# Optimization experiments

Measured on AMD Instinct MI355X. Metric: run time of the kernel, lower is better.

Reference implementation:

```python
import jax, jax.numpy as jnp
import numpy as np

T, B, I, H = 2048, 4096, 3, 5  # seq_len, batch, input_size, hidden_size (from module)


def setup_inputs() -> dict:
    key = jax.random.key(0)
    ks = jax.random.split(key, 10)
    k = 1.0 / np.sqrt(H)  # torch nn.RNN default init bound
    u = lambda kk, shape: jax.random.uniform(kk, shape, jnp.float32, -k, k)
    return {
        "x": jax.random.normal(ks[0], (T, B, I), jnp.float32),
        "hx": jax.random.normal(ks[1], (2, B, H), jnp.float32),
        "w_ih0": u(ks[2], (H, I)),
        "w_hh0": u(ks[3], (H, H)),
        "b_ih0": u(ks[4], (H,)),
        "b_hh0": u(ks[5], (H,)),
        "w_ih1": u(ks[6], (H, H)),
        "w_hh1": u(ks[7], (H, H)),
        "b_ih1": u(ks[8], (H,)),
        "b_hh1": u(ks[9], (H,)),
    }


def reference(x, hx, w_ih0, w_hh0, b_ih0, b_hh0, w_ih1, w_hh1, b_ih1, b_hh1):
    # Precompute layer-0 input projections for all timesteps in one big GEMM.
    pre0 = jnp.einsum("tbi,hi->tbh", x, w_ih0) + b_ih0  # [T, B, H]

    def step(carry, p0_t):
        h0, h1 = carry
        h0 = jnp.tanh(p0_t + h0 @ w_hh0.T + b_hh0)
        h1 = jnp.tanh(h0 @ w_ih1.T + b_ih1 + h1 @ w_hh1.T + b_hh1)
        return (h0, h1), h1

    (h0_f, h1_f), out = jax.lax.scan(step, (hx[0], hx[1]), pre0)
    h_n = jnp.stack([h0_f, h1_f])  # [2, B, H]
    return out, h_n
```

## Files before the change

### kernel.cpp

```cpp
#include <hip/hip_runtime.h>


typedef float v2f __attribute__((ext_vector_type(2)));

#define SEQ_T 2048
#define BATCH 4096
#define ISZ 3
#define HSZ 5
#define PD 8
#define XSTRIDE (BATCH * ISZ)
#define OSTRIDE (BATCH * HSZ)

template<int K>
__device__ __forceinline__ float qbcast(float v) {
    return __int_as_float(__builtin_amdgcn_mov_dpp(
        __float_as_int(v), K * 0x55, 0xF, 0xF, false));
}

__device__ __forceinline__ float tanh_fast(float a) {
    float e = __builtin_amdgcn_exp2f(a);
    return fmaf(-2.0f, __builtin_amdgcn_rcpf(1.0f + e), 1.0f);
}

__device__ __forceinline__ v2f vsplat(float s) { return (v2f){s, s}; }
__device__ __forceinline__ v2f vfma(float s, v2f w, v2f a) {
    return __builtin_elementwise_fma(vsplat(s), w, a);
}

__global__ __launch_bounds__(64, 1)
void rnn2_regs(const float* __restrict__ x, const float* __restrict__ hx,
               const float* __restrict__ w_ih0, const float* __restrict__ w_hh0,
               const float* __restrict__ b_ih0, const float* __restrict__ b_hh0,
               const float* __restrict__ w_ih1, const float* __restrict__ w_hh1,
               const float* __restrict__ b_ih1, const float* __restrict__ b_hh1,
               float* __restrict__ out)
{
    const int tid = threadIdx.x;
    const int c   = (blockIdx.x * 64 + tid) >> 2;
    const int ja  = tid & 3;
    const float S = 2.8853900817779268f;

    const v2f bias0p = (v2f){ S * (b_ih0[ja] + b_hh0[ja]), S * (b_ih0[4] + b_hh0[4]) };
    const v2f bias1p = (v2f){ S * (b_ih1[ja] + b_hh1[ja]), S * (b_ih1[4] + b_hh1[4]) };
#define LW(W, k, n)  (v2f){ S * W[ja * (n) + (k)], S * W[4 * (n) + (k)] }
    const v2f wi0p0 = LW(w_ih0, 0, ISZ), wi0p1 = LW(w_ih0, 1, ISZ), wi0p2 = LW(w_ih0, 2, ISZ);
    const v2f wh0p0 = LW(w_hh0, 0, HSZ), wh0p1 = LW(w_hh0, 1, HSZ), wh0p2 = LW(w_hh0, 2, HSZ),
              wh0p3 = LW(w_hh0, 3, HSZ), wh0p4 = LW(w_hh0, 4, HSZ);
    const v2f wi1p0 = LW(w_ih1, 0, HSZ), wi1p1 = LW(w_ih1, 1, HSZ), wi1p2 = LW(w_ih1, 2, HSZ),
              wi1p3 = LW(w_ih1, 3, HSZ), wi1p4 = LW(w_ih1, 4, HSZ);
    const v2f wh1p0 = LW(w_hh1, 0, HSZ), wh1p1 = LW(w_hh1, 1, HSZ), wh1p2 = LW(w_hh1, 2, HSZ),
              wh1p3 = LW(w_hh1, 3, HSZ), wh1p4 = LW(w_hh1, 4, HSZ);
#undef LW

    float h0b0 = hx[(size_t)c * HSZ + 0], h0b1 = hx[(size_t)c * HSZ + 1],
          h0b2 = hx[(size_t)c * HSZ + 2], h0b3 = hx[(size_t)c * HSZ + 3],
          h0b4 = hx[(size_t)c * HSZ + 4];
    const size_t hb1 = (size_t)BATCH * HSZ + (size_t)c * HSZ;
    float h1b0 = hx[hb1 + 0], h1b1 = hx[hb1 + 1], h1b2 = hx[hb1 + 2],
          h1b3 = hx[hb1 + 3], h1b4 = hx[hb1 + 4];

    unsigned xoff = (unsigned)c * ISZ;
    float x0a = x[xoff + 0*XSTRIDE], x0b = x[xoff + 0*XSTRIDE + 1], x0c = x[xoff + 0*XSTRIDE + 2];
    float x1a = x[xoff + 1*XSTRIDE], x1b = x[xoff + 1*XSTRIDE + 1], x1c = x[xoff + 1*XSTRIDE + 2];
    float x2a = x[xoff + 2*XSTRIDE], x2b = x[xoff + 2*XSTRIDE + 1], x2c = x[xoff + 2*XSTRIDE + 2];
    float x3a = x[xoff + 3*XSTRIDE], x3b = x[xoff + 3*XSTRIDE + 1], x3c = x[xoff + 3*XSTRIDE + 2];
    float x4a = x[xoff + 4*XSTRIDE], x4b = x[xoff + 4*XSTRIDE + 1], x4c = x[xoff + 4*XSTRIDE + 2];
    float x5a = x[xoff + 5*XSTRIDE], x5b = x[xoff + 5*XSTRIDE + 1], x5c = x[xoff + 5*XSTRIDE + 2];
    float x6a = x[xoff + 6*XSTRIDE], x6b = x[xoff + 6*XSTRIDE + 1], x6c = x[xoff + 6*XSTRIDE + 2];
    float x7a = x[xoff + 7*XSTRIDE], x7b = x[xoff + 7*XSTRIDE + 1], x7c = x[xoff + 7*XSTRIDE + 2];
    xoff += PD * XSTRIDE;

    unsigned ooffA = (unsigned)c * HSZ + (unsigned)ja;
    unsigned ooffB = (unsigned)c * HSZ + 4u;

#define CORE(XV0, XV1, XV2, DOLOAD)                                        \
    {                                                                      \
        const float xv0 = XV0, xv1 = XV1, xv2 = XV2;                       \
        if (DOLOAD) {                                                      \
            XV0 = x[xoff]; XV1 = x[xoff + 1]; XV2 = x[xoff + 2];           \
            xoff += XSTRIDE;                                               \
        }                                                                  \
        v2f a = bias0p, cc = (v2f){0.0f, 0.0f};                            \
        a  = vfma(xv0,  wi0p0, a);                                         \
        cc = vfma(xv1,  wi0p1, cc);                                        \
        a  = vfma(xv2,  wi0p2, a);                                         \
        cc = vfma(h0b0, wh0p0, cc);                                        \
        a  = vfma(h0b1, wh0p1, a);                                         \
        cc = vfma(h0b2, wh0p2, cc);                                        \
        a  = vfma(h0b3, wh0p3, a);                                         \
        cc = vfma(h0b4, wh0p4, cc);                                        \
        a = a + cc;                                                        \
        const float h0nA = tanh_fast(a.x);                                 \
        const float h0nB = tanh_fast(a.y);                                 \
        h0b0 = qbcast<0>(h0nA);                                            \
        h0b1 = qbcast<1>(h0nA);                                            \
        h0b2 = qbcast<2>(h0nA);                                            \
        h0b3 = qbcast<3>(h0nA);                                            \
        h0b4 = h0nB;                                                       \
        v2f d = bias1p, ee = (v2f){0.0f, 0.0f};                            \
        d  = vfma(h0b0, wi1p0, d);                                         \
        ee = vfma(h0b1, wi1p1, ee);                                        \
        d  = vfma(h0b2, wi1p2, d);                                         \
        ee = vfma(h0b3, wi1p3, ee);                                        \
        d  = vfma(h0b4, wi1p4, d);                                         \
        ee = vfma(h1b0, wh1p0, ee);                                        \
        d  = vfma(h1b1, wh1p1, d);                                         \
        ee = vfma(h1b2, wh1p2, ee);                                        \
        d  = vfma(h1b3, wh1p3, d);                                         \
        ee = vfma(h1b4, wh1p4, ee);                                        \
        d = d + ee;                                                        \
        const float h1nA = tanh_fast(d.x);                                 \
        const float h1nB = tanh_fast(d.y);                                 \
        out[ooffA] = h1nA;                                                 \
        out[ooffB] = h1nB;                                                 \
        ooffA += OSTRIDE;                                                  \
        ooffB += OSTRIDE;                                                  \
        h1b0 = qbcast<0>(h1nA);                                            \
        h1b1 = qbcast<1>(h1nA);                                            \
        h1b2 = qbcast<2>(h1nA);                                            \
        h1b3 = qbcast<3>(h1nA);                                            \
        h1b4 = h1nB;                                                       \
    }

    for (int it = 0; it < SEQ_T / PD - 1; ++it) {
        CORE(x0a, x0b, x0c, 1)
        CORE(x1a, x1b, x1c, 1)
        CORE(x2a, x2b, x2c, 1)
        CORE(x3a, x3b, x3c, 1)
        CORE(x4a, x4b, x4c, 1)
        CORE(x5a, x5b, x5c, 1)
        CORE(x6a, x6b, x6c, 1)
        CORE(x7a, x7b, x7c, 1)
    }
    CORE(x0a, x0b, x0c, 0)
    CORE(x1a, x1b, x1c, 0)
    CORE(x2a, x2b, x2c, 0)
    CORE(x3a, x3b, x3c, 0)
    CORE(x4a, x4b, x4c, 0)
    CORE(x5a, x5b, x5c, 0)
    CORE(x6a, x6b, x6c, 0)
    CORE(x7a, x7b, x7c, 0)
#undef CORE

    float* hn = out + (size_t)SEQ_T * BATCH * HSZ;
    hn[(size_t)c * HSZ + 0] = h0b0;
    hn[(size_t)c * HSZ + 1] = h0b1;
    hn[(size_t)c * HSZ + 2] = h0b2;
    hn[(size_t)c * HSZ + 3] = h0b3;
    hn[(size_t)c * HSZ + 4] = h0b4;
    hn[hb1 + 0] = h1b0;
    hn[hb1 + 1] = h1b1;
    hn[hb1 + 2] = h1b2;
    hn[hb1 + 3] = h1b3;
    hn[hb1 + 4] = h1b4;
}

extern "C" void kernel_launch(void* const* d_in, const int* in_sizes, int n_in,
                              void* d_out, int out_size, void* d_ws, size_t ws_size,
                              hipStream_t stream) {
    rnn2_regs<<<(BATCH * 4) / 64, 64, 0, stream>>>(
        (const float*)d_in[0], (const float*)d_in[1],
        (const float*)d_in[2], (const float*)d_in[3],
        (const float*)d_in[4], (const float*)d_in[5],
        (const float*)d_in[6], (const float*)d_in[7],
        (const float*)d_in[8], (const float*)d_in[9],
        (float*)d_out);
}
```

Baseline: 478.0 us.

## Pipeline RNN layers across two wavefronts via shared-memory ring buffer

Splits the two RNN layers onto separate wavefronts in a 128-thread block. Wave 0 computes layer 0 for an 8-step block and writes h0 into a double-buffered LDS ring, while wave 1 consumes the previous block to compute layer 1 and write outputs. The aim is to shorten the serial per-step dependency chain by overlapping the two layers. In exchange it adds a block barrier every 8 steps, LDS traffic, and one extra pipeline stage of latency.

```diff
diff --git a/kernel.cpp b/kernel.cpp
--- a/kernel.cpp
+++ b/kernel.cpp
@@ -7,7 +7,8 @@
 #define BATCH 4096
 #define ISZ 3
 #define HSZ 5
-#define PD 8
+#define TBLK 8
+#define NSUP (SEQ_T / TBLK)
 #define XSTRIDE (BATCH * ISZ)
 #define OSTRIDE (BATCH * HSZ)
 
@@ -16,29 +17,32 @@
     return __int_as_float(__builtin_amdgcn_mov_dpp(
         __float_as_int(v), K * 0x55, 0xF, 0xF, false));
 }
-
 __device__ __forceinline__ float tanh_fast(float a) {
     float e = __builtin_amdgcn_exp2f(a);
     return fmaf(-2.0f, __builtin_amdgcn_rcpf(1.0f + e), 1.0f);
 }
-
 __device__ __forceinline__ v2f vsplat(float s) { return (v2f){s, s}; }
 __device__ __forceinline__ v2f vfma(float s, v2f w, v2f a) {
     return __builtin_elementwise_fma(vsplat(s), w, a);
 }
 
-__global__ __launch_bounds__(64, 1)
-void rnn2_regs(const float* __restrict__ x, const float* __restrict__ hx,
-               const float* __restrict__ w_ih0, const float* __restrict__ w_hh0,
-               const float* __restrict__ b_ih0, const float* __restrict__ b_hh0,
-               const float* __restrict__ w_ih1, const float* __restrict__ w_hh1,
-               const float* __restrict__ b_ih1, const float* __restrict__ b_hh1,
-               float* __restrict__ out)
+__global__ __launch_bounds__(128, 1)
+void rnn2_ppl(const float* __restrict__ x, const float* __restrict__ hx,
+              const float* __restrict__ w_ih0, const float* __restrict__ w_hh0,
+              const float* __restrict__ b_ih0, const float* __restrict__ b_hh0,
+              const float* __restrict__ w_ih1, const float* __restrict__ w_hh1,
+              const float* __restrict__ b_ih1, const float* __restrict__ b_hh1,
+              float* __restrict__ out)
 {
-    const int tid = threadIdx.x;
-    const int c   = (blockIdx.x * 64 + tid) >> 2;
-    const int ja  = tid & 3;
-    const float S = 2.8853900817779268f;
+    __shared__ float ring[2][TBLK][16][10];
+
+    const int tid  = threadIdx.x;
+    const int wid  = tid >> 6;
+    const int lane = tid & 63;
+    const int cl   = lane >> 2;
+    const int ja   = lane & 3;
+    const int c    = blockIdx.x * 16 + cl;
+    const float S  = 2.8853900817779268f;
 
     const v2f bias0p = (v2f){ S * (b_ih0[ja] + b_hh0[ja]), S * (b_ih0[4] + b_hh0[4]) };
     const v2f bias1p = (v2f){ S * (b_ih1[ja] + b_hh1[ja]), S * (b_ih1[4] + b_hh1[4]) };
@@ -68,18 +72,16 @@
     float x5a = x[xoff + 5*XSTRIDE], x5b = x[xoff + 5*XSTRIDE + 1], x5c = x[xoff + 5*XSTRIDE + 2];
     float x6a = x[xoff + 6*XSTRIDE], x6b = x[xoff + 6*XSTRIDE + 1], x6c = x[xoff + 6*XSTRIDE + 2];
     float x7a = x[xoff + 7*XSTRIDE], x7b = x[xoff + 7*XSTRIDE + 1], x7c = x[xoff + 7*XSTRIDE + 2];
-    xoff += PD * XSTRIDE;
+    xoff += TBLK * XSTRIDE;
 
     unsigned ooffA = (unsigned)c * HSZ + (unsigned)ja;
     unsigned ooffB = (unsigned)c * HSZ + 4u;
 
-#define CORE(XV0, XV1, XV2, DOLOAD)                                        \
+#define STEP0(TT, XV0, XV1, XV2)                                           \
     {                                                                      \
         const float xv0 = XV0, xv1 = XV1, xv2 = XV2;                       \
-        if (DOLOAD) {                                                      \
-            XV0 = x[xoff]; XV1 = x[xoff + 1]; XV2 = x[xoff + 2];           \
-            xoff += XSTRIDE;                                               \
-        }                                                                  \
+        XV0 = x[xoff]; XV1 = x[xoff + 1]; XV2 = x[xoff + 2];               \
+        xoff += XSTRIDE;                                                   \
         v2f a = bias0p, cc = (v2f){0.0f, 0.0f};                            \
         a  = vfma(xv0,  wi0p0, a);                                         \
         cc = vfma(xv1,  wi0p1, cc);                                        \
@@ -90,75 +92,103 @@
         a  = vfma(h0b3, wh0p3, a);                                         \
         cc = vfma(h0b4, wh0p4, cc);                                        \
         a = a + cc;                                                        \
-        const float h0nA = tanh_fast(a.x);                                 \
-        const float h0nB = tanh_fast(a.y);                                 \
-        h0b0 = qbcast<0>(h0nA);                                            \
-        h0b1 = qbcast<1>(h0nA);                                            \
-        h0b2 = qbcast<2>(h0nA);                                            \
-        h0b3 = qbcast<3>(h0nA);                                            \
-        h0b4 = h0nB;                                                       \
+        const float nA = tanh_fast(a.x);                                   \
+        const float nB = tanh_fast(a.y);                                   \
+        h0b0 = qbcast<0>(nA);                                              \
+        h0b1 = qbcast<1>(nA);                                              \
+        h0b2 = qbcast<2>(nA);                                              \
+        h0b3 = qbcast<3>(nA);                                              \
+        h0b4 = nB;                                                         \
+        *(v2f*)&wr[TT][cl][ja * 2] = (v2f){nA, nB};                        \
+    }
+
+#define STEP1(TT, DOPRE)                                                   \
+    {                                                                      \
+        const float u0 = g0, u1 = g1, u2 = g2, u3 = g3, u4 = g4;           \
+        if (DOPRE) {                                                       \
+            const float* q = &rd[(TT) + 1][cl][0];                         \
+            g0 = q[0]; g1 = q[2]; g2 = q[4]; g3 = q[6]; g4 = q[1];         \
+        }                                                                  \
         v2f d = bias1p, ee = (v2f){0.0f, 0.0f};                            \
-        d  = vfma(h0b0, wi1p0, d);                                         \
-        ee = vfma(h0b1, wi1p1, ee);                                        \
-        d  = vfma(h0b2, wi1p2, d);                                         \
-        ee = vfma(h0b3, wi1p3, ee);                                        \
-        d  = vfma(h0b4, wi1p4, d);                                         \
+        d  = vfma(u0,   wi1p0, d);                                         \
+        ee = vfma(u1,   wi1p1, ee);                                        \
+        d  = vfma(u2,   wi1p2, d);                                         \
+        ee = vfma(u3,   wi1p3, ee);                                        \
+        d  = vfma(u4,   wi1p4, d);                                         \
         ee = vfma(h1b0, wh1p0, ee);                                        \
         d  = vfma(h1b1, wh1p1, d);                                         \
         ee = vfma(h1b2, wh1p2, ee);                                        \
         d  = vfma(h1b3, wh1p3, d);                                         \
         ee = vfma(h1b4, wh1p4, ee);                                        \
         d = d + ee;                                                        \
-        const float h1nA = tanh_fast(d.x);                                 \
-        const float h1nB = tanh_fast(d.y);                                 \
-        out[ooffA] = h1nA;                                                 \
-        out[ooffB] = h1nB;                                                 \
+        const float nA = tanh_fast(d.x);                                   \
+        const float nB = tanh_fast(d.y);                                   \
+        out[ooffA] = nA;                                                   \
+        out[ooffB] = nB;                                                   \
         ooffA += OSTRIDE;                                                  \
         ooffB += OSTRIDE;                                                  \
-        h1b0 = qbcast<0>(h1nA);                                            \
-        h1b1 = qbcast<1>(h1nA);                                            \
-        h1b2 = qbcast<2>(h1nA);                                            \
-        h1b3 = qbcast<3>(h1nA);                                            \
-        h1b4 = h1nB;                                                       \
+        h1b0 = qbcast<0>(nA);                                              \
+        h1b1 = qbcast<1>(nA);                                              \
+        h1b2 = qbcast<2>(nA);                                              \
+        h1b3 = qbcast<3>(nA);                                              \
+        h1b4 = nB;                                                         \
     }
 
-    for (int it = 0; it < SEQ_T / PD - 1; ++it) {
-        CORE(x0a, x0b, x0c, 1)
-        CORE(x1a, x1b, x1c, 1)
-        CORE(x2a, x2b, x2c, 1)
-        CORE(x3a, x3b, x3c, 1)
-        CORE(x4a, x4b, x4c, 1)
-        CORE(x5a, x5b, x5c, 1)
-        CORE(x6a, x6b, x6c, 1)
-        CORE(x7a, x7b, x7c, 1)
+    for (int si = 0; si <= NSUP; ++si) {
+        __syncthreads();
+        if (wid == 0) {
+            if (si < NSUP) {
+                if (si == NSUP - 1) xoff -= (unsigned)(TBLK * XSTRIDE);
+                float (*wr)[16][10] = ring[si & 1];
+                STEP0(0, x0a, x0b, x0c)
+                STEP0(1, x1a, x1b, x1c)
+                STEP0(2, x2a, x2b, x2c)
+                STEP0(3, x3a, x3b, x3c)
+                STEP0(4, x4a, x4b, x4c)
+                STEP0(5, x5a, x5b, x5c)
+                STEP0(6, x6a, x6b, x6c)
+                STEP0(7, x7a, x7b, x7c)
+            }
+        } else {
+            if (si > 0) {
+                float (*rd)[16][10] = ring[(si - 1) & 1];
+                float g0, g1, g2, g3, g4;
+                { const float* q = &rd[0][cl][0];
+                  g0 = q[0]; g1 = q[2]; g2 = q[4]; g3 = q[6]; g4 = q[1]; }
+                STEP1(0, 1)
+                STEP1(1, 1)
+                STEP1(2, 1)
+                STEP1(3, 1)
+                STEP1(4, 1)
+                STEP1(5, 1)
+                STEP1(6, 1)
+                STEP1(7, 0)
+            }
+        }
     }
-    CORE(x0a, x0b, x0c, 0)
-    CORE(x1a, x1b, x1c, 0)
-    CORE(x2a, x2b, x2c, 0)
-    CORE(x3a, x3b, x3c, 0)
-    CORE(x4a, x4b, x4c, 0)
-    CORE(x5a, x5b, x5c, 0)
-    CORE(x6a, x6b, x6c, 0)
-    CORE(x7a, x7b, x7c, 0)
-#undef CORE
+#undef STEP0
+#undef STEP1
 
     float* hn = out + (size_t)SEQ_T * BATCH * HSZ;
-    hn[(size_t)c * HSZ + 0] = h0b0;
-    hn[(size_t)c * HSZ + 1] = h0b1;
-    hn[(size_t)c * HSZ + 2] = h0b2;
-    hn[(size_t)c * HSZ + 3] = h0b3;
-    hn[(size_t)c * HSZ + 4] = h0b4;
-    hn[hb1 + 0] = h1b0;
-    hn[hb1 + 1] = h1b1;
-    hn[hb1 + 2] = h1b2;
-    hn[hb1 + 3] = h1b3;
-    hn[hb1 + 4] = h1b4;
+    if (wid == 0) {
+        hn[(size_t)c * HSZ + 0] = h0b0;
+        hn[(size_t)c * HSZ + 1] = h0b1;
+        hn[(size_t)c * HSZ + 2] = h0b2;
+        hn[(size_t)c * HSZ + 3] = h0b3;
+        hn[(size_t)c * HSZ + 4] = h0b4;
+    } else {
+        hn[hb1 + 0] = h1b0;
+        hn[hb1 + 1] = h1b1;
+        hn[hb1 + 2] = h1b2;
+        hn[hb1 + 3] = h1b3;
+        hn[hb1 + 4] = h1b4;
+    }
 }
 
 extern "C" void kernel_launch(void* const* d_in, const int* in_sizes, int n_in,
                               void* d_out, int out_size, void* d_ws, size_t ws_size,
                               hipStream_t stream) {
-    rnn2_regs<<<(BATCH * 4) / 64, 64, 0, stream>>>(
+    rnn2_ppl<<<BATCH / 16, 128, 0, stream>>>(
         (const float*)d_in[0], (const float*)d_in[1],
         (const float*)d_in[2], (const float*)d_in[3],
         (const float*)d_in[4], (const float*)d_in[5],
```

After: 535.1 us. 11.9% more time.

## Software-pipeline the two RNN layers across timesteps to shorten the dependency chain

Applied to the files above, without the earlier changes.

Layer 1 of step t-1 is now computed in the same block as layer 0 of step t, since both depend only on h0 from step t-1. This interleaves two independent FMA, exp and rcp chains per iteration and roughly halves the serial critical path per timestep. A prologue runs layer 0 alone and an epilogue finishes the last layer-1 step. Register pressure rises somewhat from the extra live accumulators.

```diff
diff --git a/kernel.cpp b/kernel.cpp
--- a/kernel.cpp
+++ b/kernel.cpp
@@ -7,7 +7,6 @@
 #define BATCH 4096
 #define ISZ 3
 #define HSZ 5
-#define PD 8
 #define XSTRIDE (BATCH * ISZ)
 #define OSTRIDE (BATCH * HSZ)
 
@@ -16,24 +15,18 @@
     return __int_as_float(__builtin_amdgcn_mov_dpp(
         __float_as_int(v), K * 0x55, 0xF, 0xF, false));
 }
-
-__device__ __forceinline__ float tanh_fast(float a) {
-    float e = __builtin_amdgcn_exp2f(a);
-    return fmaf(-2.0f, __builtin_amdgcn_rcpf(1.0f + e), 1.0f);
-}
-
 __device__ __forceinline__ v2f vsplat(float s) { return (v2f){s, s}; }
 __device__ __forceinline__ v2f vfma(float s, v2f w, v2f a) {
     return __builtin_elementwise_fma(vsplat(s), w, a);
 }
 
 __global__ __launch_bounds__(64, 1)
-void rnn2_regs(const float* __restrict__ x, const float* __restrict__ hx,
-               const float* __restrict__ w_ih0, const float* __restrict__ w_hh0,
-               const float* __restrict__ b_ih0, const float* __restrict__ b_hh0,
-               const float* __restrict__ w_ih1, const float* __restrict__ w_hh1,
-               const float* __restrict__ b_ih1, const float* __restrict__ b_hh1,
-               float* __restrict__ out)
+void rnn2_swp(const float* __restrict__ x, const float* __restrict__ hx,
+              const float* __restrict__ w_ih0, const float* __restrict__ w_hh0,
+              const float* __restrict__ b_ih0, const float* __restrict__ b_hh0,
+              const float* __restrict__ w_ih1, const float* __restrict__ w_hh1,
+              const float* __restrict__ b_ih1, const float* __restrict__ b_hh1,
+              float* __restrict__ out)
 {
     const int tid = threadIdx.x;
     const int c   = (blockIdx.x * 64 + tid) >> 2;
@@ -68,18 +61,69 @@
     float x5a = x[xoff + 5*XSTRIDE], x5b = x[xoff + 5*XSTRIDE + 1], x5c = x[xoff + 5*XSTRIDE + 2];
     float x6a = x[xoff + 6*XSTRIDE], x6b = x[xoff + 6*XSTRIDE + 1], x6c = x[xoff + 6*XSTRIDE + 2];
     float x7a = x[xoff + 7*XSTRIDE], x7b = x[xoff + 7*XSTRIDE + 1], x7c = x[xoff + 7*XSTRIDE + 2];
-    xoff += PD * XSTRIDE;
+    xoff += 8 * XSTRIDE;
 
     unsigned ooffA = (unsigned)c * HSZ + (unsigned)ja;
     unsigned ooffB = (unsigned)c * HSZ + 4u;
 
-#define CORE(XV0, XV1, XV2, DOLOAD)                                        \
+#define PAIR(XV0, XV1, XV2, DOLOAD)                                        \
     {                                                                      \
         const float xv0 = XV0, xv1 = XV1, xv2 = XV2;                       \
         if (DOLOAD) {                                                      \
             XV0 = x[xoff]; XV1 = x[xoff + 1]; XV2 = x[xoff + 2];           \
             xoff += XSTRIDE;                                               \
         }                                                                  \
+        v2f a = bias0p, cc = (v2f){0.0f, 0.0f};                            \
+        v2f d = bias1p, ee = (v2f){0.0f, 0.0f};                            \
+        a  = vfma(xv0,  wi0p0, a);                                         \
+        d  = vfma(h0b0, wi1p0, d);                                         \
+        cc = vfma(xv1,  wi0p1, cc);                                        \
+        ee = vfma(h0b1, wi1p1, ee);                                        \
+        a  = vfma(xv2,  wi0p2, a);                                         \
+        d  = vfma(h0b2, wi1p2, d);                                         \
+        cc = vfma(h0b0, wh0p0, cc);                                        \
+        ee = vfma(h0b3, wi1p3, ee);                                        \
+        a  = vfma(h0b1, wh0p1, a);                                         \
+        d  = vfma(h0b4, wi1p4, d);                                         \
+        cc = vfma(h0b2, wh0p2, cc);                                        \
+        ee = vfma(h1b0, wh1p0, ee);                                        \
+        a  = vfma(h0b3, wh0p3, a);                                         \
+        d  = vfma(h1b1, wh1p1, d);                                         \
+        cc = vfma(h0b4, wh0p4, cc);                                        \
+        ee = vfma(h1b2, wh1p2, ee);                                        \
+        a = a + cc;                                                        \
+        d  = vfma(h1b3, wh1p3, d);                                         \
+        ee = vfma(h1b4, wh1p4, ee);                                        \
+        const float e0x = __builtin_amdgcn_exp2f(a.x);                     \
+        const float e0y = __builtin_amdgcn_exp2f(a.y);                     \
+        d = d + ee;                                                        \
+        const float e1x = __builtin_amdgcn_exp2f(d.x);                     \
+        const float e1y = __builtin_amdgcn_exp2f(d.y);                     \
+        const float n0A = fmaf(-2.0f, __builtin_amdgcn_rcpf(1.0f + e0x), 1.0f); \
+        const float n0B = fmaf(-2.0f, __builtin_amdgcn_rcpf(1.0f + e0y), 1.0f); \
+        const float n1A = fmaf(-2.0f, __builtin_amdgcn_rcpf(1.0f + e1x), 1.0f); \
+        const float n1B = fmaf(-2.0f, __builtin_amdgcn_rcpf(1.0f + e1y), 1.0f); \
+        h0b0 = qbcast<0>(n0A);                                             \
+        h0b1 = qbcast<1>(n0A);                                             \
+        h0b2 = qbcast<2>(n0A);                                             \
+        h0b3 = qbcast<3>(n0A);                                             \
+        h0b4 = n0B;                                                        \
+        out[ooffA] = n1A;                                                  \
+        out[ooffB] = n1B;                                                  \
+        ooffA += OSTRIDE;                                                  \
+        ooffB += OSTRIDE;                                                  \
+        h1b0 = qbcast<0>(n1A);                                             \
+        h1b1 = qbcast<1>(n1A);                                             \
+        h1b2 = qbcast<2>(n1A);                                             \
+        h1b3 = qbcast<3>(n1A);                                             \
+        h1b4 = n1B;                                                        \
+    }
+
+#define P0ONLY(XV0, XV1, XV2)                                              \
+    {                                                                      \
+        const float xv0 = XV0, xv1 = XV1, xv2 = XV2;                       \
+        XV0 = x[xoff]; XV1 = x[xoff + 1]; XV2 = x[xoff + 2];               \
+        xoff += XSTRIDE;                                                   \
         v2f a = bias0p, cc = (v2f){0.0f, 0.0f};                            \
         a  = vfma(xv0,  wi0p0, a);                                         \
         cc = vfma(xv1,  wi0p1, cc);                                        \
@@ -90,57 +134,73 @@
         a  = vfma(h0b3, wh0p3, a);                                         \
         cc = vfma(h0b4, wh0p4, cc);                                        \
         a = a + cc;                                                        \
-        const float h0nA = tanh_fast(a.x);                                 \
-        const float h0nB = tanh_fast(a.y);                                 \
-        h0b0 = qbcast<0>(h0nA);                                            \
-        h0b1 = qbcast<1>(h0nA);                                            \
-        h0b2 = qbcast<2>(h0nA);                                            \
-        h0b3 = qbcast<3>(h0nA);                                            \
-        h0b4 = h0nB;                                                       \
-        v2f d = bias1p, ee = (v2f){0.0f, 0.0f};                            \
-        d  = vfma(h0b0, wi1p0, d);                                         \
-        ee = vfma(h0b1, wi1p1, ee);                                        \
-        d  = vfma(h0b2, wi1p2, d);                                         \
-        ee = vfma(h0b3, wi1p3, ee);                                        \
-        d  = vfma(h0b4, wi1p4, d);                                         \
-        ee = vfma(h1b0, wh1p0, ee);                                        \
-        d  = vfma(h1b1, wh1p1, d);                                         \
-        ee = vfma(h1b2, wh1p2, ee);                                        \
-        d  = vfma(h1b3, wh1p3, d);                                         \
-        ee = vfma(h1b4, wh1p4, ee);                                        \
-        d = d + ee;                                                        \
-        const float h1nA = tanh_fast(d.x);                                 \
-        const float h1nB = tanh_fast(d.y);                                 \
-        out[ooffA] = h1nA;                                                 \
-        out[ooffB] = h1nB;                                                 \
-        ooffA += OSTRIDE;                                                  \
-        ooffB += OSTRIDE;                                                  \
-        h1b0 = qbcast<0>(h1nA);                                            \
-        h1b1 = qbcast<1>(h1nA);                                            \
-        h1b2 = qbcast<2>(h1nA);                                            \
-        h1b3 = qbcast<3>(h1nA);                                            \
-        h1b4 = h1nB;                                                       \
-    }
-
-    for (int it = 0; it < SEQ_T / PD - 1; ++it) {
-        CORE(x0a, x0b, x0c, 1)
-        CORE(x1a, x1b, x1c, 1)
-        CORE(x2a, x2b, x2c, 1)
-        CORE(x3a, x3b, x3c, 1)
-        CORE(x4a, x4b, x4c, 1)
-        CORE(x5a, x5b, x5c, 1)
-        CORE(x6a, x6b, x6c, 1)
-        CORE(x7a, x7b, x7c, 1)
-    }
-    CORE(x0a, x0b, x0c, 0)
-    CORE(x1a, x1b, x1c, 0)
-    CORE(x2a, x2b, x2c, 0)
-    CORE(x3a, x3b, x3c, 0)
-    CORE(x4a, x4b, x4c, 0)
-    CORE(x5a, x5b, x5c, 0)
-    CORE(x6a, x6b, x6c, 0)
-    CORE(x7a, x7b, x7c, 0)
-#undef CORE
+        const float e0x = __builtin_amdgcn_exp2f(a.x);                     \
+        const float e0y = __builtin_amdgcn_exp2f(a.y);                     \
+        const float n0A = fmaf(-2.0f, __builtin_amdgcn_rcpf(1.0f + e0x), 1.0f); \
+        const float n0B = fmaf(-2.0f, __builtin_amdgcn_rcpf(1.0f + e0y), 1.0f); \
+        h0b0 = qbcast<0>(n0A);                                             \
+        h0b1 = qbcast<1>(n0A);                                             \
+        h0b2 = qbcast<2>(n0A);                                             \
+        h0b3 = qbcast<3>(n0A);                                             \
+        h0b4 = n0B;                                                        \
+    }
+
+    P0ONLY(x0a, x0b, x0c)
+    PAIR(x1a, x1b, x1c, 1)
+    PAIR(x2a, x2b, x2c, 1)
+    PAIR(x3a, x3b, x3c, 1)
+    PAIR(x4a, x4b, x4c, 1)
+    PAIR(x5a, x5b, x5c, 1)
+    PAIR(x6a, x6b, x6c, 1)
+    PAIR(x7a, x7b, x7c, 1)
+
+    for (int blk = 1; blk < SEQ_T / 8 - 1; ++blk) {
+        PAIR(x0a, x0b, x0c, 1)
+        PAIR(x1a, x1b, x1c, 1)
+        PAIR(x2a, x2b, x2c, 1)
+        PAIR(x3a, x3b, x3c, 1)
+        PAIR(x4a, x4b, x4c, 1)
+        PAIR(x5a, x5b, x5c, 1)
+        PAIR(x6a, x6b, x6c, 1)
+        PAIR(x7a, x7b, x7c, 1)
+    }
+
+    PAIR(x0a, x0b, x0c, 0)
+    PAIR(x1a, x1b, x1c, 0)
+    PAIR(x2a, x2b, x2c, 0)
+    PAIR(x3a, x3b, x3c, 0)
+    PAIR(x4a, x4b, x4c, 0)
+    PAIR(x5a, x5b, x5c, 0)
+    PAIR(x6a, x6b, x6c, 0)
+    PAIR(x7a, x7b, x7c, 0)
+
+    {
+        v2f d = bias1p, ee = (v2f){0.0f, 0.0f};
+        d  = vfma(h0b0, wi1p0, d);
+        ee = vfma(h0b1, wi1p1, ee);
+        d  = vfma(h0b2, wi1p2, d);
+        ee = vfma(h0b3, wi1p3, ee);
+        d  = vfma(h0b4, wi1p4, d);
+        ee = vfma(h1b0, wh1p0, ee);
+        d  = vfma(h1b1, wh1p1, d);
+        ee = vfma(h1b2, wh1p2, ee);
+        d  = vfma(h1b3, wh1p3, d);
+        ee = vfma(h1b4, wh1p4, ee);
+        d = d + ee;
+        const float e1x = __builtin_amdgcn_exp2f(d.x);
+        const float e1y = __builtin_amdgcn_exp2f(d.y);
+        const float n1A = fmaf(-2.0f, __builtin_amdgcn_rcpf(1.0f + e1x), 1.0f);
+        const float n1B = fmaf(-2.0f, __builtin_amdgcn_rcpf(1.0f + e1y), 1.0f);
+        out[ooffA] = n1A;
+        out[ooffB] = n1B;
+        h1b0 = qbcast<0>(n1A);
+        h1b1 = qbcast<1>(n1A);
+        h1b2 = qbcast<2>(n1A);
+        h1b3 = qbcast<3>(n1A);
+        h1b4 = n1B;
+    }
+#undef PAIR
+#undef P0ONLY
 
     float* hn = out + (size_t)SEQ_T * BATCH * HSZ;
     hn[(size_t)c * HSZ + 0] = h0b0;
@@ -158,7 +218,7 @@
 extern "C" void kernel_launch(void* const* d_in, const int* in_sizes, int n_in,
                               void* d_out, int out_size, void* d_ws, size_t ws_size,
                               hipStream_t stream) {
-    rnn2_regs<<<(BATCH * 4) / 64, 64, 0, stream>>>(
+    rnn2_swp<<<(BATCH * 4) / 64, 64, 0, stream>>>(
         (const float*)d_in[0], (const float*)d_in[1],
         (const float*)d_in[2], (const float*)d_in[3],
         (const float*)d_in[4], (const float*)d_in[5],
```

Result: faster. 446.0 us (-6.7%).
